# Optimization experiments

Hardware: AMD Instinct MI355X
Metric: run time of the kernel (lower is better)

## Reference

```python
import jax, jax.numpy as jnp
import numpy as np

N = 50000          # nodes
E = 600000         # edges
D = 128            # g_dim = h1_dim = h2_dim
R = 8              # 2 * n_speakers**2, n_speakers=2
B = 10             # num_bases


def setup_inputs() -> dict:
    key = jax.random.key(0)
    ks = jax.random.split(key, 10)
    s = 1.0 / np.sqrt(D)
    return {
        "node_features": jax.random.normal(ks[0], (N, D), jnp.float32),
        "edge_index": jax.random.randint(ks[1], (2, E), 0, N, jnp.int64),
        "edge_type": jax.random.randint(ks[2], (E,), 0, R, jnp.int64),
        # RGCNConv params (basis decomposition)
        "basis": jax.random.normal(ks[3], (B, D, D), jnp.float32) * s,
        "comp": jax.random.normal(ks[4], (R, B), jnp.float32) * (1.0 / np.sqrt(B)),
        "root": jax.random.normal(ks[5], (D, D), jnp.float32) * s,
        "bias1": jnp.zeros((D,), jnp.float32),
        # GraphConv params
        "w_rel": jax.random.normal(ks[6], (D, D), jnp.float32) * s,
        "b_rel": jnp.zeros((D,), jnp.float32),
        "w_root": jax.random.normal(ks[7], (D, D), jnp.float32) * s,
    }


def reference(node_features, edge_index, edge_type, basis, comp, root, bias1, w_rel, b_rel, w_root):
    x = node_features
    n = x.shape[0]
    r = comp.shape[0]
    src, dst = edge_index[0], edge_index[1]

    # ---- RGCNConv (basis decomposition, per-relation mean aggregation) ----
    # project through bases once: [N, B, D]
    xb = jnp.einsum('ni,bio->nbo', x, basis)
    # per-edge message: combine bases with relation coefficients  [E, D]
    msg = jnp.einsum('eb,ebo->eo', comp[edge_type], xb[src])
    # per-(dst, relation) mean normalization
    seg = dst * r + edge_type                       # [E]
    cnt = jax.ops.segment_sum(jnp.ones((msg.shape[0],), x.dtype), seg, num_segments=n * r)
    norm = 1.0 / jnp.maximum(cnt[seg], 1.0)         # [E]
    agg = jax.ops.segment_sum(msg * norm[:, None], dst, num_segments=n)  # [N, D]
    h1 = agg + x @ root + bias1

    # ---- GraphConv (add aggregation of neighbors + root transform) ----
    nbr = jax.ops.segment_sum(h1[src], dst, num_segments=n)  # [N, D]
    out = nbr @ w_rel.T + b_rel + h1 @ w_root.T
    return out
```

## Files before the change

kernel.cpp:

```cpp
#include <hip/hip_runtime.h>
#include <stdint.h>

#define N_NODES 50000
#define E_EDGES 600000
#define D 128
#define R_REL 8
#define B_BASES 10
#define RN (R_REL * N_NODES)

typedef __attribute__((ext_vector_type(8))) short bf16x8;
typedef __attribute__((ext_vector_type(4))) float f32x4;

__device__ __forceinline__ short f2b(float f) {
    uint32_t u = __float_as_uint(f);
    u += 0x7fff + ((u >> 16) & 1);
    return (short)(u >> 16);
}
__device__ __forceinline__ float b2f(uint16_t u) {
    return __uint_as_float((uint32_t)u << 16);
}

__device__ __forceinline__ void lds_barrier() {
    __builtin_amdgcn_sched_barrier(0);
    asm volatile("s_waitcnt lgkmcnt(0)\n\ts_barrier" ::: "memory");
    __builtin_amdgcn_sched_barrier(0);
}

__global__ __launch_bounds__(256) void k_front(const float* __restrict__ x,
                                               unsigned short* __restrict__ xb,
                                               const int* __restrict__ dst,
                                               const int* __restrict__ et,
                                               int* __restrict__ cntr,
                                               const float* __restrict__ basis,
                                               const float* __restrict__ comp,
                                               const float* __restrict__ root,
                                               const float* __restrict__ wrel,
                                               const float* __restrict__ wroot,
                                               short* __restrict__ wt,
                                               short* __restrict__ wrel_b,
                                               short* __restrict__ wroot_b) {
    const int XB_N = N_NODES * D / 8;
    int tid = blockIdx.x * 256 + threadIdx.x;
    if (tid < XB_N) {
        const float4* s = (const float4*)x + (size_t)tid * 2;
        float4 v0 = s[0], v1 = s[1];
        union { uint4 u; unsigned short h[8]; } pk;
        pk.h[0] = (unsigned short)f2b(v0.x); pk.h[1] = (unsigned short)f2b(v0.y);
        pk.h[2] = (unsigned short)f2b(v0.z); pk.h[3] = (unsigned short)f2b(v0.w);
        pk.h[4] = (unsigned short)f2b(v1.x); pk.h[5] = (unsigned short)f2b(v1.y);
        pk.h[6] = (unsigned short)f2b(v1.z); pk.h[7] = (unsigned short)f2b(v1.w);
        ((uint4*)xb)[tid] = pk.u;
    } else if (tid < XB_N + E_EDGES) {
        int e = tid - XB_N;
        atomicAdd(&cntr[dst[e] * R_REL + et[e]], 1);
    } else {
        int t2 = tid - XB_N - E_EDGES;
        if (t2 < 9 * D * D) {
            int s = t2 >> 14;
            int rem = t2 & 16383;
            int j = rem >> 7, i = rem & 127;
            float v;
            if (s < 8) {
                v = 0.f;
#pragma unroll
                for (int b = 0; b < B_BASES; b++)
                    v += comp[s * B_BASES + b] * basis[b * D * D + i * D + j];
            } else {
                v = root[i * D + j];
            }
            wt[t2] = f2b(v);
        } else {
            int t3 = t2 - 9 * D * D;
            if (t3 < D * D) {
                wrel_b[t3]  = f2b(wrel[t3]);
                wroot_b[t3] = f2b(wroot[t3]);
            }
        }
    }
}

__device__ __forceinline__ int wave_scan_incl(int v) {
    int lane = threadIdx.x & 63;
#pragma unroll
    for (int off = 1; off < 64; off <<= 1) {
        int n = __shfl_up(v, off, 64);
        if (lane >= off) v += n;
    }
    return v;
}

__global__ __launch_bounds__(1024) void k_scan_a(const int* __restrict__ in,
                                                 int* __restrict__ out,
                                                 int* __restrict__ bsum, int n) {
    __shared__ int wsum[16];
    int t = threadIdx.x, lane = t & 63, wid = t >> 6;
    int g = blockIdx.x * 1024 + t;
    int v = (g < n) ? in[g] : 0;
    int isc = wave_scan_incl(v);
    if (lane == 63) wsum[wid] = isc;
    __syncthreads();
    if (wid == 0) {
        int wv = (lane < 16) ? wsum[lane] : 0;
        int wsc = wave_scan_incl(wv);
        if (lane < 16) wsum[lane] = wsc - wv;
    }
    __syncthreads();
    if (g < n) out[g] = wsum[wid] + isc - v;
    if (t == 1023 && bsum) bsum[blockIdx.x] = wsum[15] + isc;
}

__global__ __launch_bounds__(1024) void k_scan_c(int* __restrict__ out,
                                                 const int* __restrict__ bsum, int n) {
    int g = blockIdx.x * 1024 + threadIdx.x;
    if (g < n) out[g] += bsum[blockIdx.x];
}

__global__ __launch_bounds__(256) void k_bucket(const int* __restrict__ src,
                                                const int* __restrict__ dst,
                                                const int* __restrict__ et,
                                                int* __restrict__ seg_off,
                                                int* __restrict__ es1) {
    int e = blockIdx.x * 256 + threadIdx.x;
    if (e >= E_EDGES) return;
    int key = dst[e] * R_REL + et[e];
    int pos = atomicAdd(&seg_off[key], 1);
    es1[pos] = src[e];
}

__global__ __launch_bounds__(256) void k_aggmean(const unsigned short* __restrict__ xb,
                                                 const int* __restrict__ es1,
                                                 const int* __restrict__ seg_off,
                                                 unsigned short* __restrict__ mx) {
    int t = threadIdx.x;
    int sw = t >> 4, l = t & 15;
    int k = blockIdx.x * 16 + sw;
    if (k >= RN) return;
    int start = (k == 0) ? 0 : seg_off[k - 1];
    int end = seg_off[k];
    float ax[8];
#pragma unroll
    for (int q = 0; q < 8; q++) ax[q] = 0.f;
    size_t loff = (size_t)l * 8;
    int pos = start;
    for (; pos + 2 <= end; pos += 2) {
        int s0 = es1[pos], s1 = es1[pos + 1];
        uint4 v0 = *(const uint4*)(xb + (size_t)s0 * D + loff);
        uint4 v1 = *(const uint4*)(xb + (size_t)s1 * D + loff);
        const uint32_t* w0 = (const uint32_t*)&v0;
        const uint32_t* w1 = (const uint32_t*)&v1;
#pragma unroll
        for (int q = 0; q < 4; q++) {
            ax[q * 2]     += b2f((uint16_t)w0[q]) + b2f((uint16_t)w1[q]);
            ax[q * 2 + 1] += b2f((uint16_t)(w0[q] >> 16)) + b2f((uint16_t)(w1[q] >> 16));
        }
    }
    if (pos < end) {
        int s0 = es1[pos];
        uint4 v0 = *(const uint4*)(xb + (size_t)s0 * D + loff);
        const uint32_t* w0 = (const uint32_t*)&v0;
#pragma unroll
        for (int q = 0; q < 4; q++) {
            ax[q * 2]     += b2f((uint16_t)w0[q]);
            ax[q * 2 + 1] += b2f((uint16_t)(w0[q] >> 16));
        }
    }
    float nm = (end > start) ? 1.f / (float)(end - start) : 0.f;
    union { uint4 u; unsigned short h[8]; } pk;
#pragma unroll
    for (int q = 0; q < 8; q++) pk.h[q] = (unsigned short)f2b(ax[q] * nm);
    *(uint4*)(mx + (size_t)k * D + loff) = pk.u;
}

__global__ __launch_bounds__(256) void k_h1_gemm(const unsigned short* __restrict__ mx,
                                                 const unsigned short* __restrict__ xb,
                                                 const short* __restrict__ wt,
                                                 const float* __restrict__ bias1,
                                                 unsigned short* __restrict__ h1b) {
    __shared__ short ws[2][128 * 128];
    int t = threadIdx.x;
    int wave = t >> 6, lane = t & 63, quad = lane >> 4, l16 = lane & 15;
    int base = blockIdx.x * 128;
    int n0 = base + wave * 32 + l16;
    int n1 = n0 + 16;
    int nc0 = n0 < N_NODES ? n0 : N_NODES - 1;
    int nc1 = n1 < N_NODES ? n1 : N_NODES - 1;
    int ci0 = wave * 8;

    auto aptr = [&](int nc, int s) -> const unsigned short* {
        return (s < 8) ? mx + ((size_t)nc * 8 + s) * D : xb + (size_t)nc * D;
    };

    uint4 aReg[2][2][4];
    {
        uint4 b0[8];
#pragma unroll
        for (int i = 0; i < 8; i++) {
            int row = (ci0 + i) * 4 + quad;
            b0[i] = *(const uint4*)(wt + row * D + (l16 << 3));
        }
#pragma unroll
        for (int kc = 0; kc < 4; kc++) {
            int co = (kc * 4 + quad) * 8;
            aReg[0][0][kc] = *(const uint4*)(aptr(nc0, 0) + co);
            aReg[0][1][kc] = *(const uint4*)(aptr(nc1, 0) + co);
            aReg[1][0][kc] = *(const uint4*)(aptr(nc0, 1) + co);
            aReg[1][1][kc] = *(const uint4*)(aptr(nc1, 1) + co);
        }
#pragma unroll
        for (int i = 0; i < 8; i++) {
            int row = (ci0 + i) * 4 + quad;
            *(uint4*)&ws[0][row * 128 + ((l16 ^ (row & 15)) << 3)] = b0[i];
        }
    }
    lds_barrier();

    f32x4 acc[2][8];
#pragma unroll
    for (int tl = 0; tl < 2; tl++)
#pragma unroll
        for (int jt = 0; jt < 8; jt++) acc[tl][jt] = (f32x4){0.f, 0.f, 0.f, 0.f};

    for (int s = 0; s < 9; s++) {
        int cur = s & 1;
        uint4 bn[8];
        if (s + 1 < 9) {
            const short* wb = wt + (size_t)(s + 1) * D * D;
#pragma unroll
            for (int i = 0; i < 8; i++) {
                int row = (ci0 + i) * 4 + quad;
                bn[i] = *(const uint4*)(wb + row * D + (l16 << 3));
            }
        }
#pragma unroll
        for (int kc = 0; kc < 4; kc++) {
            int c0 = kc * 4 + quad;
            bf16x8 a0 = *(bf16x8*)&aReg[cur][0][kc];
            bf16x8 a1 = *(bf16x8*)&aReg[cur][1][kc];
#pragma unroll
            for (int jt = 0; jt < 8; jt++) {
                bf16x8 b = *(const bf16x8*)&ws[cur][(jt * 16 + l16) * 128 + ((c0 ^ l16) << 3)];
                acc[0][jt] = __builtin_amdgcn_mfma_f32_16x16x32_bf16(a0, b, acc[0][jt], 0, 0, 0);
                acc[1][jt] = __builtin_amdgcn_mfma_f32_16x16x32_bf16(a1, b, acc[1][jt], 0, 0, 0);
            }
        }
        if (s + 2 <= 8) {
#pragma unroll
            for (int kc = 0; kc < 4; kc++) {
                int co = (kc * 4 + quad) * 8;
                aReg[cur][0][kc] = *(const uint4*)(aptr(nc0, s + 2) + co);
                aReg[cur][1][kc] = *(const uint4*)(aptr(nc1, s + 2) + co);
            }
        }
        if (s + 1 < 9) {
#pragma unroll
            for (int i = 0; i < 8; i++) {
                int row = (ci0 + i) * 4 + quad;
                *(uint4*)&ws[cur ^ 1][row * 128 + ((l16 ^ (row & 15)) << 3)] = bn[i];
            }
        }
        lds_barrier();
    }

#pragma unroll
    for (int tl = 0; tl < 2; tl++) {
#pragma unroll
        for (int reg = 0; reg < 4; reg++) {
            int node = base + wave * 32 + tl * 16 + quad * 4 + reg;
            if (node >= N_NODES) continue;
#pragma unroll
            for (int jt = 0; jt < 8; jt++) {
                int col = jt * 16 + l16;
                float v = acc[tl][jt][reg] + bias1[col];
                h1b[(size_t)node * D + col] = (unsigned short)f2b(v);
            }
        }
    }
}

__global__ __launch_bounds__(256) void k_agg_nbr(const unsigned short* __restrict__ h1b,
                                                 const int* __restrict__ es1,
                                                 const int* __restrict__ seg_off,
                                                 unsigned short* __restrict__ nbr) {
    int t = threadIdx.x;
    int wave = t >> 6, lane = t & 63, sub = lane >> 4, l = lane & 15;
    int d = blockIdx.x * 16 + wave * 4 + sub;
    if (d >= N_NODES) return;
    int start = (d == 0) ? 0 : seg_off[d * R_REL - 1];
    int end = seg_off[d * R_REL + 7];
    float acc[8];
#pragma unroll
    for (int j = 0; j < 8; j++) acc[j] = 0.f;
    size_t loff = (size_t)l * 8;

    int pos = start;
    for (; pos + 4 <= end; pos += 4) {
        int i0 = es1[pos], i1 = es1[pos + 1], i2 = es1[pos + 2], i3 = es1[pos + 3];
        uint4 v0 = *(const uint4*)(h1b + (size_t)i0 * D + loff);
        uint4 v1 = *(const uint4*)(h1b + (size_t)i1 * D + loff);
        uint4 v2 = *(const uint4*)(h1b + (size_t)i2 * D + loff);
        uint4 v3 = *(const uint4*)(h1b + (size_t)i3 * D + loff);
        const uint32_t* w0 = (const uint32_t*)&v0;
        const uint32_t* w1 = (const uint32_t*)&v1;
        const uint32_t* w2 = (const uint32_t*)&v2;
        const uint32_t* w3 = (const uint32_t*)&v3;
#pragma unroll
        for (int q = 0; q < 4; q++) {
            acc[q * 2]     += b2f((uint16_t)w0[q]) + b2f((uint16_t)w1[q]) +
                              b2f((uint16_t)w2[q]) + b2f((uint16_t)w3[q]);
            acc[q * 2 + 1] += b2f((uint16_t)(w0[q] >> 16)) + b2f((uint16_t)(w1[q] >> 16)) +
                              b2f((uint16_t)(w2[q] >> 16)) + b2f((uint16_t)(w3[q] >> 16));
        }
    }
    for (; pos < end; pos++) {
        int i0 = es1[pos];
        uint4 v0 = *(const uint4*)(h1b + (size_t)i0 * D + loff);
        const uint32_t* w0 = (const uint32_t*)&v0;
#pragma unroll
        for (int q = 0; q < 4; q++) {
            acc[q * 2]     += b2f((uint16_t)w0[q]);
            acc[q * 2 + 1] += b2f((uint16_t)(w0[q] >> 16));
        }
    }

    union { uint4 u; unsigned short h[8]; } pk;
#pragma unroll
    for (int j = 0; j < 8; j++) pk.h[j] = (unsigned short)f2b(acc[j]);
    *(uint4*)(nbr + (size_t)d * D + loff) = pk.u;
}

__global__ __launch_bounds__(256) void k_out2(const unsigned short* __restrict__ h1b,
                                              const unsigned short* __restrict__ nbr,
                                              const short* __restrict__ wroot_b,
                                              const short* __restrict__ wrel_b,
                                              const float* __restrict__ brel,
                                              float* __restrict__ out) {
    __shared__ short ws[2][128 * 128];
    int t = threadIdx.x;
    int wave = t >> 6, lane = t & 63, quad = lane >> 4, l16 = lane & 15;
    int base = blockIdx.x * 128;
    int n0 = base + wave * 32 + l16;
    int n1 = n0 + 16;
    int nc0 = n0 < N_NODES ? n0 : N_NODES - 1;
    int nc1 = n1 < N_NODES ? n1 : N_NODES - 1;
    int ci0 = wave * 8;

    uint4 aReg[2][2][4];
    {
        uint4 b0[8];
#pragma unroll
        for (int i = 0; i < 8; i++) {
            int row = (ci0 + i) * 4 + quad;
            b0[i] = *(const uint4*)(wroot_b + row * D + (l16 << 3));
        }
#pragma unroll
        for (int kc = 0; kc < 4; kc++) {
            int co = (kc * 4 + quad) * 8;
            aReg[0][0][kc] = *(const uint4*)(h1b + (size_t)nc0 * D + co);
            aReg[0][1][kc] = *(const uint4*)(h1b + (size_t)nc1 * D + co);
            aReg[1][0][kc] = *(const uint4*)(nbr + (size_t)nc0 * D + co);
            aReg[1][1][kc] = *(const uint4*)(nbr + (size_t)nc1 * D + co);
        }
#pragma unroll
        for (int i = 0; i < 8; i++) {
            int row = (ci0 + i) * 4 + quad;
            *(uint4*)&ws[0][row * 128 + ((l16 ^ (row & 15)) << 3)] = b0[i];
        }
    }
    __syncthreads();

    f32x4 acc[2][8];
#pragma unroll
    for (int tl = 0; tl < 2; tl++)
#pragma unroll
        for (int jt = 0; jt < 8; jt++) acc[tl][jt] = (f32x4){0.f, 0.f, 0.f, 0.f};

#pragma unroll
    for (int s = 0; s < 2; s++) {
        int cur = s & 1;
        uint4 bn[8];
        if (s == 0) {
#pragma unroll
            for (int i = 0; i < 8; i++) {
                int row = (ci0 + i) * 4 + quad;
                bn[i] = *(const uint4*)(wrel_b + row * D + (l16 << 3));
            }
        }
#pragma unroll
        for (int kc = 0; kc < 4; kc++) {
            int c0 = kc * 4 + quad;
            bf16x8 a0 = *(bf16x8*)&aReg[cur][0][kc];
            bf16x8 a1 = *(bf16x8*)&aReg[cur][1][kc];
#pragma unroll
            for (int jt = 0; jt < 8; jt++) {
                bf16x8 b = *(const bf16x8*)&ws[cur][(jt * 16 + l16) * 128 + ((c0 ^ l16) << 3)];
                acc[0][jt] = __builtin_amdgcn_mfma_f32_16x16x32_bf16(a0, b, acc[0][jt], 0, 0, 0);
                acc[1][jt] = __builtin_amdgcn_mfma_f32_16x16x32_bf16(a1, b, acc[1][jt], 0, 0, 0);
            }
        }
        if (s == 0) {
#pragma unroll
            for (int i = 0; i < 8; i++) {
                int row = (ci0 + i) * 4 + quad;
                *(uint4*)&ws[1][row * 128 + ((l16 ^ (row & 15)) << 3)] = bn[i];
            }
            __syncthreads();
        }
    }

#pragma unroll
    for (int tl = 0; tl < 2; tl++) {
#pragma unroll
        for (int reg = 0; reg < 4; reg++) {
            int node = base + wave * 32 + tl * 16 + quad * 4 + reg;
            if (node >= N_NODES) continue;
#pragma unroll
            for (int jt = 0; jt < 8; jt++) {
                int col = jt * 16 + l16;
                out[(size_t)node * D + col] = acc[tl][jt][reg] + brel[col];
            }
        }
    }
}

extern "C" void kernel_launch(void* const* d_in, const int* in_sizes, int n_in,
                              void* d_out, int out_size, void* d_ws, size_t ws_size,
                              hipStream_t stream) {
    const float* x     = (const float*)d_in[0];
    const int*   ei    = (const int*)d_in[1];
    const int*   et    = (const int*)d_in[2];
    const float* basis = (const float*)d_in[3];
    const float* comp  = (const float*)d_in[4];
    const float* root  = (const float*)d_in[5];
    const float* bias1 = (const float*)d_in[6];
    const float* wrel  = (const float*)d_in[7];
    const float* brel  = (const float*)d_in[8];
    const float* wroot = (const float*)d_in[9];
    float* out = (float*)d_out;
    const int* src = ei;
    const int* dst = ei + E_EDGES;

    char* p = (char*)d_ws;
    auto alloc = [&](size_t bytes) { char* q = p; p += (bytes + 255) & ~(size_t)255; return q; };
    short* wt      = (short*)alloc((size_t)9 * D * D * sizeof(short));
    short* wrel_b  = (short*)alloc(D * D * sizeof(short));
    short* wroot_b = (short*)alloc(D * D * sizeof(short));
    int*   cntr    = (int*)alloc((size_t)RN * sizeof(int));
    int*   seg_off = (int*)alloc((size_t)RN * sizeof(int));
    int*   es1     = (int*)alloc((size_t)(E_EDGES + 16) * sizeof(int));
    int*   bsum    = (int*)alloc(1024 * sizeof(int));
    unsigned short* xb  = (unsigned short*)alloc((size_t)N_NODES * D * sizeof(unsigned short));
    unsigned short* mx  = (unsigned short*)alloc((size_t)RN * D * sizeof(unsigned short));
    unsigned short* h1b = (unsigned short*)alloc((size_t)N_NODES * D * sizeof(unsigned short));
    unsigned short* nbr = xb;

    hipMemsetAsync(cntr, 0, (size_t)RN * sizeof(int), stream);

    const int XB_N = N_NODES * D / 8;
    int nfront = (XB_N + E_EDGES + 9 * D * D + D * D + 255) / 256;
    k_front<<<nfront, 256, 0, stream>>>(x, xb, dst, et, cntr,
                                        basis, comp, root, wrel, wroot,
                                        wt, wrel_b, wroot_b);

    int nscan = (RN + 1023) / 1024;
    k_scan_a<<<nscan, 1024, 0, stream>>>(cntr, seg_off, bsum, RN);
    k_scan_a<<<1, 1024, 0, stream>>>(bsum, bsum, nullptr, nscan);
    k_scan_c<<<nscan, 1024, 0, stream>>>(seg_off, bsum, RN);

    k_bucket<<<(E_EDGES + 255) / 256, 256, 0, stream>>>(src, dst, et, seg_off, es1);

    k_aggmean<<<RN / 16, 256, 0, stream>>>(xb, es1, seg_off, mx);

    int nb2 = (N_NODES + 127) / 128;
    int na = (N_NODES + 15) / 16;
    k_h1_gemm<<<nb2, 256, 0, stream>>>(mx, xb, wt, bias1, h1b);
    k_agg_nbr<<<na, 256, 0, stream>>>(h1b, es1, seg_off, nbr);
    k_out2<<<nb2, 256, 0, stream>>>(h1b, nbr, wroot_b, wrel_b, brel, out);
}
```

Baseline: 265.0 us.

## Fuse per-relation mean aggregation into the h1 GEMM A-fragment loads

Removes the separate k_aggmean kernel and its [R*N, D] bf16 intermediate buffer. The h1 GEMM kernel now gathers neighbor rows and computes the per-(dst, relation) mean directly into MFMA A fragments for each relation step. This cuts a large global write and read of the intermediate plus one launch. In exchange, gather latency now sits inside the GEMM loop without the previous register double-buffered prefetch, and only 16 lanes' worth of rows per wave issue gathers, so load-level parallelism may drop.

```diff
diff --git a/kernel.cpp b/kernel.cpp
--- a/kernel.cpp
+++ b/kernel.cpp
@@ -24,6 +24,55 @@
     __builtin_amdgcn_sched_barrier(0);
     asm volatile("s_waitcnt lgkmcnt(0)\n\ts_barrier" ::: "memory");
     __builtin_amdgcn_sched_barrier(0);
+}
+
+__device__ __forceinline__ void gather_mean_frag(const unsigned short* __restrict__ xb,
+                                                 const int* __restrict__ es1,
+                                                 int st, int en, int quad,
+                                                 bf16x8* afrag) {
+    float m[4][8];
+#pragma unroll
+    for (int kc = 0; kc < 4; kc++)
+#pragma unroll
+        for (int q = 0; q < 8; q++) m[kc][q] = 0.f;
+    int pos = st;
+    for (; pos + 2 <= en; pos += 2) {
+        const unsigned short* r0 = xb + (size_t)es1[pos] * D + quad * 8;
+        const unsigned short* r1 = xb + (size_t)es1[pos + 1] * D + quad * 8;
+#pragma unroll
+        for (int kc = 0; kc < 4; kc++) {
+            uint4 g0 = *(const uint4*)(r0 + kc * 32);
+            uint4 g1 = *(const uint4*)(r1 + kc * 32);
+            const uint32_t* w0 = (const uint32_t*)&g0;
+            const uint32_t* w1 = (const uint32_t*)&g1;
+#pragma unroll
+            for (int q = 0; q < 4; q++) {
+                m[kc][q * 2]     += b2f((uint16_t)w0[q]) + b2f((uint16_t)w1[q]);
+                m[kc][q * 2 + 1] += b2f((uint16_t)(w0[q] >> 16)) + b2f((uint16_t)(w1[q] >> 16));
+            }
+        }
+    }
+    if (pos < en) {
+        const unsigned short* r0 = xb + (size_t)es1[pos] * D + quad * 8;
+#pragma unroll
+        for (int kc = 0; kc < 4; kc++) {
+            uint4 g0 = *(const uint4*)(r0 + kc * 32);
+            const uint32_t* w0 = (const uint32_t*)&g0;
+#pragma unroll
+            for (int q = 0; q < 4; q++) {
+                m[kc][q * 2]     += b2f((uint16_t)w0[q]);
+                m[kc][q * 2 + 1] += b2f((uint16_t)(w0[q] >> 16));
+            }
+        }
+    }
+    float nm = (en > st) ? 1.f / (float)(en - st) : 0.f;
+#pragma unroll
+    for (int kc = 0; kc < 4; kc++) {
+        union { uint4 u; unsigned short h[8]; } pk;
+#pragma unroll
+        for (int q = 0; q < 8; q++) pk.h[q] = (unsigned short)f2b(m[kc][q] * nm);
+        afrag[kc] = *(bf16x8*)&pk.u;
+    }
 }
 
 __global__ __launch_bounds__(256) void k_front(const float* __restrict__ x,
@@ -127,55 +176,12 @@
     es1[pos] = src[e];
 }
 
-__global__ __launch_bounds__(256) void k_aggmean(const unsigned short* __restrict__ xb,
-                                                 const int* __restrict__ es1,
-                                                 const int* __restrict__ seg_off,
-                                                 unsigned short* __restrict__ mx) {
-    int t = threadIdx.x;
-    int sw = t >> 4, l = t & 15;
-    int k = blockIdx.x * 16 + sw;
-    if (k >= RN) return;
-    int start = (k == 0) ? 0 : seg_off[k - 1];
-    int end = seg_off[k];
-    float ax[8];
-#pragma unroll
-    for (int q = 0; q < 8; q++) ax[q] = 0.f;
-    size_t loff = (size_t)l * 8;
-    int pos = start;
-    for (; pos + 2 <= end; pos += 2) {
-        int s0 = es1[pos], s1 = es1[pos + 1];
-        uint4 v0 = *(const uint4*)(xb + (size_t)s0 * D + loff);
-        uint4 v1 = *(const uint4*)(xb + (size_t)s1 * D + loff);
-        const uint32_t* w0 = (const uint32_t*)&v0;
-        const uint32_t* w1 = (const uint32_t*)&v1;
-#pragma unroll
-        for (int q = 0; q < 4; q++) {
-            ax[q * 2]     += b2f((uint16_t)w0[q]) + b2f((uint16_t)w1[q]);
-            ax[q * 2 + 1] += b2f((uint16_t)(w0[q] >> 16)) + b2f((uint16_t)(w1[q] >> 16));
-        }
-    }
-    if (pos < end) {
-        int s0 = es1[pos];
-        uint4 v0 = *(const uint4*)(xb + (size_t)s0 * D + loff);
-        const uint32_t* w0 = (const uint32_t*)&v0;
-#pragma unroll
-        for (int q = 0; q < 4; q++) {
-            ax[q * 2]     += b2f((uint16_t)w0[q]);
-            ax[q * 2 + 1] += b2f((uint16_t)(w0[q] >> 16));
-        }
-    }
-    float nm = (end > start) ? 1.f / (float)(end - start) : 0.f;
-    union { uint4 u; unsigned short h[8]; } pk;
-#pragma unroll
-    for (int q = 0; q < 8; q++) pk.h[q] = (unsigned short)f2b(ax[q] * nm);
-    *(uint4*)(mx + (size_t)k * D + loff) = pk.u;
-}
-
-__global__ __launch_bounds__(256) void k_h1_gemm(const unsigned short* __restrict__ mx,
-                                                 const unsigned short* __restrict__ xb,
-                                                 const short* __restrict__ wt,
-                                                 const float* __restrict__ bias1,
-                                                 unsigned short* __restrict__ h1b) {
+__global__ __launch_bounds__(256) void k_h1_fused(const unsigned short* __restrict__ xb,
+                                                  const int* __restrict__ es1,
+                                                  const int* __restrict__ seg_off,
+                                                  const short* __restrict__ wt,
+                                                  const float* __restrict__ bias1,
+                                                  unsigned short* __restrict__ h1b) {
     __shared__ short ws[2][128 * 128];
     int t = threadIdx.x;
     int wave = t >> 6, lane = t & 63, quad = lane >> 4, l16 = lane & 15;
@@ -186,25 +192,12 @@
     int nc1 = n1 < N_NODES ? n1 : N_NODES - 1;
     int ci0 = wave * 8;
 
-    auto aptr = [&](int nc, int s) -> const unsigned short* {
-        return (s < 8) ? mx + ((size_t)nc * 8 + s) * D : xb + (size_t)nc * D;
-    };
-
-    uint4 aReg[2][2][4];
     {
         uint4 b0[8];
 #pragma unroll
         for (int i = 0; i < 8; i++) {
             int row = (ci0 + i) * 4 + quad;
             b0[i] = *(const uint4*)(wt + row * D + (l16 << 3));
-        }
-#pragma unroll
-        for (int kc = 0; kc < 4; kc++) {
-            int co = (kc * 4 + quad) * 8;
-            aReg[0][0][kc] = *(const uint4*)(aptr(nc0, 0) + co);
-            aReg[0][1][kc] = *(const uint4*)(aptr(nc1, 0) + co);
-            aReg[1][0][kc] = *(const uint4*)(aptr(nc0, 1) + co);
-            aReg[1][1][kc] = *(const uint4*)(aptr(nc1, 1) + co);
         }
 #pragma unroll
         for (int i = 0; i < 8; i++) {
@@ -231,24 +224,32 @@
                 bn[i] = *(const uint4*)(wb + row * D + (l16 << 3));
             }
         }
+        bf16x8 a0[4], a1[4];
+        if (s < 8) {
+            int k0 = nc0 * R_REL + s;
+            int st0 = (k0 == 0) ? 0 : seg_off[k0 - 1];
+            int en0 = seg_off[k0];
+            int k1 = nc1 * R_REL + s;
+            int st1 = seg_off[k1 - 1];
+            int en1 = seg_off[k1];
+            gather_mean_frag(xb, es1, st0, en0, quad, a0);
+            gather_mean_frag(xb, es1, st1, en1, quad, a1);
+        } else {
+#pragma unroll
+            for (int kc = 0; kc < 4; kc++) {
+                int co = (kc * 4 + quad) * 8;
+                a0[kc] = *(const bf16x8*)(xb + (size_t)nc0 * D + co);
+                a1[kc] = *(const bf16x8*)(xb + (size_t)nc1 * D + co);
+            }
+        }
 #pragma unroll
         for (int kc = 0; kc < 4; kc++) {
             int c0 = kc * 4 + quad;
-            bf16x8 a0 = *(bf16x8*)&aReg[cur][0][kc];
-            bf16x8 a1 = *(bf16x8*)&aReg[cur][1][kc];
 #pragma unroll
             for (int jt = 0; jt < 8; jt++) {
                 bf16x8 b = *(const bf16x8*)&ws[cur][(jt * 16 + l16) * 128 + ((c0 ^ l16) << 3)];
-                acc[0][jt] = __builtin_amdgcn_mfma_f32_16x16x32_bf16(a0, b, acc[0][jt], 0, 0, 0);
-                acc[1][jt] = __builtin_amdgcn_mfma_f32_16x16x32_bf16(a1, b, acc[1][jt], 0, 0, 0);
-            }
-        }
-        if (s + 2 <= 8) {
-#pragma unroll
-            for (int kc = 0; kc < 4; kc++) {
-                int co = (kc * 4 + quad) * 8;
-                aReg[cur][0][kc] = *(const uint4*)(aptr(nc0, s + 2) + co);
-                aReg[cur][1][kc] = *(const uint4*)(aptr(nc1, s + 2) + co);
+                acc[0][jt] = __builtin_amdgcn_mfma_f32_16x16x32_bf16(a0[kc], b, acc[0][jt], 0, 0, 0);
+                acc[1][jt] = __builtin_amdgcn_mfma_f32_16x16x32_bf16(a1[kc], b, acc[1][jt], 0, 0, 0);
             }
         }
         if (s + 1 < 9) {
@@ -449,7 +450,6 @@
     int*   es1     = (int*)alloc((size_t)(E_EDGES + 16) * sizeof(int));
     int*   bsum    = (int*)alloc(1024 * sizeof(int));
     unsigned short* xb  = (unsigned short*)alloc((size_t)N_NODES * D * sizeof(unsigned short));
-    unsigned short* mx  = (unsigned short*)alloc((size_t)RN * D * sizeof(unsigned short));
     unsigned short* h1b = (unsigned short*)alloc((size_t)N_NODES * D * sizeof(unsigned short));
     unsigned short* nbr = xb;
 
@@ -468,11 +468,9 @@
 
     k_bucket<<<(E_EDGES + 255) / 256, 256, 0, stream>>>(src, dst, et, seg_off, es1);
 
-    k_aggmean<<<RN / 16, 256, 0, stream>>>(xb, es1, seg_off, mx);
-
     int nb2 = (N_NODES + 127) / 128;
     int na = (N_NODES + 15) / 16;
-    k_h1_gemm<<<nb2, 256, 0, stream>>>(mx, xb, wt, bias1, h1b);
+    k_h1_fused<<<nb2, 256, 0, stream>>>(xb, es1, seg_off, wt, bias1, h1b);
     k_agg_nbr<<<na, 256, 0, stream>>>(h1b, es1, seg_off, nbr);
     k_out2<<<nb2, 256, 0, stream>>>(h1b, nbr, wroot_b, wrel_b, brel, out);
 }
```

New measurement: 296.7 us. +12.0%, slower.
